# Optimization experiments

Hardware: AMD Instinct MI355X
Metric: run time of the kernel (lower is better)

Reference implementation:

```python
import jax, jax.numpy as jnp
import numpy as np

TEMPERATURE = 0.5
SCALE_LOSS = 1.0 / 32.0
LAMBDA = 0.0039


def setup_inputs() -> dict:
    key = jax.random.key(0)
    z = jax.random.normal(key, (4096, 6, 256), dtype=jnp.float32)
    return {"z": z}


def reference(z):
    B, V = z.shape[0], z.shape[1]
    # [B, V, ...] -> [V, B, D], L2-normalize embeddings
    zv = z.reshape(B, V, -1).transpose(1, 0, 2)
    zn = zv / jnp.linalg.norm(zv, axis=-1, keepdims=True)

    # Positive error: per-sample cross-view similarity [B, V, V]
    sim_pos = jnp.einsum('vbd,wbd->bvw', zn, zn)
    pos = jnp.exp((1.0 - sim_pos) / TEMPERATURE).mean(axis=(1, 2))  # [B]

    # Negative error: per-view within-batch similarity [V, B, B]
    sim_neg = jnp.exp(jnp.einsum('vbd,vcd->vbc', zn, zn) / TEMPERATURE)
    offdiag_mask = ~jnp.eye(B, dtype=bool)  # [B, B]
    off_mean = jnp.where(offdiag_mask[None], sim_neg, 0.0).sum(-1) / (B - 1)  # [V, B]
    neg = off_mean.sum(0)  # [B], accumulated over views

    return jnp.sum(pos) * SCALE_LOSS + LAMBDA * jnp.sum(neg)
```

## Files before the change

### kernel.cpp

```cpp
#include <hip/hip_runtime.h>
#include <cstdint>
#include <cstddef>

#define B_N 4096
#define V_N 6
#define D_N 256
#define CHUNK 8
#define NCHUNK 80
#define NGRAM (NCHUNK * V_N)
#define NPOSB 1024

typedef int i32x4 __attribute__((ext_vector_type(4)));

#define QC 298.0f
#define INV_C2_X2 (2.0f / (QC * QC))

__device__ __forceinline__ void async_load16(void* lds, const void* gmem) {
  __builtin_amdgcn_global_load_lds(
      (const __attribute__((address_space(1))) unsigned int*)gmem,
      (__attribute__((address_space(3))) unsigned int*)lds,
      16, 0, 0);
}

__global__ __launch_bounds__(256) void norm_pos_kernel(
    const float* __restrict__ z, signed char* __restrict__ znb,
    float* __restrict__ pos_blk, int* __restrict__ done) {
  const int lane = threadIdx.x & 63;
  const int w = threadIdx.x >> 6;
  const int b = blockIdx.x * 4 + w;
  __shared__ float red[4];

  if (blockIdx.x == 0 && threadIdx.x == 0) *done = 0;

  const float4* zb4 = (const float4*)(z + (size_t)b * (V_N * D_N));
  float4 x[V_N];
#pragma unroll
  for (int v = 0; v < V_N; ++v) x[v] = zb4[v * 64 + lane];

  float s[21];
  {
    int p = 0;
#pragma unroll
    for (int v = 0; v < V_N; ++v)
#pragma unroll
      for (int u = v; u < V_N; ++u) {
        s[p] = x[v].x * x[u].x + x[v].y * x[u].y +
               x[v].z * x[u].z + x[v].w * x[u].w;
        ++p;
      }
  }
#pragma unroll
  for (int off = 1; off < 64; off <<= 1)
#pragma unroll
    for (int q = 0; q < 21; ++q)
      s[q] += __shfl_xor(s[q], off);

  const int selfidx[V_N] = {0, 6, 11, 15, 18, 20};
  float inv[V_N];
#pragma unroll
  for (int v = 0; v < V_N; ++v) inv[v] = rsqrtf(s[selfidx[v]]);

#pragma unroll
  for (int v = 0; v < V_N; ++v) {
    const float sc = inv[v] * QC;
    int q0 = (int)rintf(fminf(127.0f, fmaxf(-127.0f, x[v].x * sc)));
    int q1 = (int)rintf(fminf(127.0f, fmaxf(-127.0f, x[v].y * sc)));
    int q2 = (int)rintf(fminf(127.0f, fmaxf(-127.0f, x[v].z * sc)));
    int q3 = (int)rintf(fminf(127.0f, fmaxf(-127.0f, x[v].w * sc)));
    int packed = (q0 & 255) | ((q1 & 255) << 8) | ((q2 & 255) << 16)
               | ((q3 & 255) << 24);
    ((int*)(znb + ((size_t)v * B_N + b) * D_N))[lane] = packed;
  }

  float psum = 0.0f;
  {
    int p = 0;
#pragma unroll
    for (int v = 0; v < V_N; ++v)
#pragma unroll
      for (int u = v; u < V_N; ++u) {
        if (u > v) psum += __expf(2.0f * (1.0f - s[p] * inv[v] * inv[u]));
        ++p;
      }
  }
  if (lane == 0) red[w] = psum;
  __syncthreads();
  if (threadIdx.x == 0)
    pos_blk[blockIdx.x] = red[0] + red[1] + red[2] + red[3];
}

__global__ __launch_bounds__(256, 2) void gram_kernel(
    const signed char* __restrict__ znb, const float* __restrict__ pos_blk,
    float* __restrict__ neg_blk, int* __restrict__ done,
    float* __restrict__ out) {
  const int v = blockIdx.y;
  const int bid = blockIdx.y * NCHUNK + blockIdx.x;

  int i = 31, rem = blockIdx.x;
  for (int r = 31; r >= 0; --r) {
    const int nc = (r + 8) >> 3;
    if (rem < nc) { i = r; break; }
    rem -= nc;
  }
  const int j0 = rem * CHUNK;
  const int jend = min(j0 + CHUNK, i + 1);
  const int nsteps = 2 * (jend - j0);

  const signed char* Zv = znb + (size_t)v * B_N * D_N;
  const signed char* Ag = Zv + (size_t)(i * 128) * D_N;

  __shared__ signed char As[128][256];
  __shared__ signed char Bs[2][128][128];
  __shared__ float red[4];
  __shared__ int lastblk;

  const int tid = threadIdx.x;
  const int lane = tid & 63;
  const int w = tid >> 6;
  const int wr = w >> 1;
  const int wc = w & 1;
  const int kc = lane >> 4;
  const int mrow = wr * 64 + (lane & 15);
  const int ncol = wc * 64 + (lane & 15);

  signed char* AsF = &As[0][0];

#pragma unroll
  for (int q = 0; q < 8; ++q) {
    const int sA = tid + 256 * q;
    const int row = sA >> 4;
    const int gc = (sA & 15) ^ (row & 15);
    async_load16(AsF + sA * 16, Ag + (size_t)row * D_N + gc * 16);
  }
#pragma unroll
  for (int st = 0; st < 2; ++st) {
    if (st < nsteps) {
      const int jn = j0 + (st >> 1), hn = st & 1;
      const signed char* Bg = Zv + (size_t)(jn * 128) * D_N + hn * 128;
      signed char* BsF = &Bs[st & 1][0][0];
#pragma unroll
      for (int q = 0; q < 4; ++q) {
        const int s = tid + 256 * q;
        const int row = s >> 3;
        const int gc = (s & 7) ^ (row & 7);
        async_load16(BsF + s * 16, Bg + (size_t)row * D_N + gc * 16);
      }
    }
  }
  asm volatile("s_waitcnt vmcnt(4)" ::: "memory");
  __builtin_amdgcn_sched_barrier(0);
  __builtin_amdgcn_s_barrier();

  float wsum = 0.0f;
  int s = 0;
  for (int jt = j0; jt < jend; ++jt) {
    i32x4 c[4][4];
#pragma unroll
    for (int a = 0; a < 4; ++a)
#pragma unroll
      for (int b2 = 0; b2 < 4; ++b2) c[a][b2] = (i32x4){0, 0, 0, 0};

#pragma unroll
    for (int h = 0; h < 2; ++h, ++s) {
      const signed char* BsF = &Bs[s & 1][0][0];
      __builtin_amdgcn_s_setprio(1);
#pragma unroll
      for (int kk = 0; kk < 2; ++kk) {
        const int cb8 = kk * 4 + kc;
        const int ca16 = h * 8 + kk * 4 + kc;
        i32x4 af[4], bfr[4];
#pragma unroll
        for (int f = 0; f < 4; ++f) {
          const int ra = mrow + 16 * f;
          const int rb = ncol + 16 * f;
          af[f]  = *(const i32x4*)(AsF + ra * 256 + ((ca16 ^ (ra & 15)) * 16));
          bfr[f] = *(const i32x4*)(BsF + rb * 128 + ((cb8 ^ (rb & 7)) * 16));
        }
#pragma unroll
        for (int fm = 0; fm < 4; ++fm)
#pragma unroll
          for (int fn = 0; fn < 4; ++fn)
            c[fm][fn] = __builtin_amdgcn_mfma_i32_16x16x64_i8(
                af[fm], bfr[fn], c[fm][fn], 0, 0, 0);
      }
      __builtin_amdgcn_s_setprio(0);
      __builtin_amdgcn_s_barrier();
      const int sn = s + 2;
      if (sn < nsteps) {
        const int jn = j0 + (sn >> 1), hn = sn & 1;
        const signed char* Bg = Zv + (size_t)(jn * 128) * D_N + hn * 128;
        signed char* BsN = &Bs[s & 1][0][0];
#pragma unroll
        for (int q = 0; q < 4; ++q) {
          const int sg = tid + 256 * q;
          const int row = sg >> 3;
          const int gc = (sg & 7) ^ (row & 7);
          async_load16(BsN + sg * 16, Bg + (size_t)row * D_N + gc * 16);
        }
      }
      if (h == 1) {
        float tsum = 0.0f;
        if (i != jt) {
#pragma unroll
          for (int fm = 0; fm < 4; ++fm)
#pragma unroll
            for (int fn = 0; fn < 4; ++fn)
#pragma unroll
              for (int r = 0; r < 4; ++r)
                tsum += __expf((float)c[fm][fn][r] * INV_C2_X2);
          wsum += 2.0f * tsum;
        } else {
          const int rb0 = wr * 64 + (lane >> 4) * 4;
          const int cb0 = wc * 64 + (lane & 15);
#pragma unroll
          for (int fm = 0; fm < 4; ++fm)
#pragma unroll
            for (int fn = 0; fn < 4; ++fn) {
              const int gcol = cb0 + fn * 16;
#pragma unroll
              for (int r = 0; r < 4; ++r) {
                const int grow = rb0 + fm * 16 + r;
                float e = __expf((float)c[fm][fn][r] * INV_C2_X2);
                tsum += (grow == gcol) ? 0.0f : e;
              }
            }
          wsum += tsum;
        }
      }
      if (sn < nsteps) {
        asm volatile("s_waitcnt vmcnt(4)" ::: "memory");
      } else {
        asm volatile("s_waitcnt vmcnt(0)" ::: "memory");
      }
      __builtin_amdgcn_sched_barrier(0);
      __builtin_amdgcn_s_barrier();
    }
  }

#pragma unroll
  for (int off = 32; off > 0; off >>= 1) wsum += __shfl_down(wsum, off);
  if (lane == 0) red[w] = wsum;
  __syncthreads();
  if (tid == 0) {
    neg_blk[bid] = red[0] + red[1] + red[2] + red[3];
    __threadfence();
    lastblk = (atomicAdd(done, 1) == NGRAM - 1) ? 1 : 0;
  }
  __syncthreads();

  if (lastblk) {
    float p = 0.0f, n = 0.0f;
    for (int idx = tid; idx < NPOSB; idx += 256) p += pos_blk[idx];
    for (int idx = tid; idx < NGRAM; idx += 256)
      n += __hip_atomic_load(&neg_blk[idx], __ATOMIC_RELAXED,
                             __HIP_MEMORY_SCOPE_AGENT);
#pragma unroll
    for (int off = 32; off > 0; off >>= 1) {
      p += __shfl_down(p, off);
      n += __shfl_down(n, off);
    }
    __shared__ float pr[4], nr[4];
    if (lane == 0) { pr[w] = p; nr[w] = n; }
    __syncthreads();
    if (tid == 0) {
      float P = pr[0] + pr[1] + pr[2] + pr[3];
      float N = nr[0] + nr[1] + nr[2] + nr[3];
      out[0] = (1.0f / 32.0f) * ((float)B_N / 6.0f + P / 18.0f) +
               0.0039f * (N / (float)(B_N - 1));
    }
  }
}

extern "C" void kernel_launch(void* const* d_in, const int* in_sizes, int n_in,
                              void* d_out, int out_size, void* d_ws, size_t ws_size,
                              hipStream_t stream) {
  const float* z = (const float*)d_in[0];
  float* out = (float*)d_out;
  float* pos_blk = (float*)d_ws;
  float* neg_blk = (float*)((char*)d_ws + 8192);
  int* done = (int*)((char*)d_ws + 16384);
  signed char* znb = (signed char*)((char*)d_ws + 32768);

  norm_pos_kernel<<<NPOSB, 256, 0, stream>>>(z, znb, pos_blk, done);
  dim3 grid(NCHUNK, V_N, 1);
  gram_kernel<<<grid, 256, 0, stream>>>(znb, pos_blk, neg_blk, done, out);
}
```

Before: 108.5 us.

## Fuse normalize and gram kernels into one persistent kernel with grid barrier

Merges the normalization/positive-term kernel and the int8 gram kernel into a single launch of 480 blocks. Each block does a grid-strided share of normalization, then waits on a global atomic barrier before running its gram tile. Monotonic device counters replace the per-launch reset. This removes a kernel launch and the gap between the two kernels, but requires all 480 blocks to be co-resident (2 per CU) or the barrier deadlocks. The first phase now runs with fewer blocks and more iterations each.

```diff
diff --git a/kernel.cpp b/kernel.cpp
--- a/kernel.cpp
+++ b/kernel.cpp
@@ -8,12 +8,14 @@
 #define CHUNK 8
 #define NCHUNK 80
 #define NGRAM (NCHUNK * V_N)
-#define NPOSB 1024
 
 typedef int i32x4 __attribute__((ext_vector_type(4)));
 
 #define QC 298.0f
 #define INV_C2_X2 (2.0f / (QC * QC))
+
+__device__ int g_bar = 0;
+__device__ int g_fin = 0;
 
 __device__ __forceinline__ void async_load16(void* lds, const void* gmem) {
   __builtin_amdgcn_global_load_lds(
@@ -22,81 +24,94 @@
       16, 0, 0);
 }
 
-__global__ __launch_bounds__(256) void norm_pos_kernel(
+__global__ __launch_bounds__(256, 2) void mega_kernel(
     const float* __restrict__ z, signed char* __restrict__ znb,
-    float* __restrict__ pos_blk, int* __restrict__ done) {
-  const int lane = threadIdx.x & 63;
-  const int w = threadIdx.x >> 6;
-  const int b = blockIdx.x * 4 + w;
+    float* __restrict__ pos_blk, float* __restrict__ neg_blk,
+    float* __restrict__ out) {
+  __shared__ signed char As[128][256];
+  __shared__ signed char Bs[2][128][128];
   __shared__ float red[4];
-
-  if (blockIdx.x == 0 && threadIdx.x == 0) *done = 0;
-
-  const float4* zb4 = (const float4*)(z + (size_t)b * (V_N * D_N));
-  float4 x[V_N];
-#pragma unroll
-  for (int v = 0; v < V_N; ++v) x[v] = zb4[v * 64 + lane];
-
-  float s[21];
-  {
-    int p = 0;
-#pragma unroll
-    for (int v = 0; v < V_N; ++v)
-#pragma unroll
-      for (int u = v; u < V_N; ++u) {
-        s[p] = x[v].x * x[u].x + x[v].y * x[u].y +
-               x[v].z * x[u].z + x[v].w * x[u].w;
-        ++p;
-      }
-  }
-#pragma unroll
-  for (int off = 1; off < 64; off <<= 1)
-#pragma unroll
-    for (int q = 0; q < 21; ++q)
-      s[q] += __shfl_xor(s[q], off);
-
-  const int selfidx[V_N] = {0, 6, 11, 15, 18, 20};
-  float inv[V_N];
-#pragma unroll
-  for (int v = 0; v < V_N; ++v) inv[v] = rsqrtf(s[selfidx[v]]);
-
-#pragma unroll
-  for (int v = 0; v < V_N; ++v) {
-    const float sc = inv[v] * QC;
-    int q0 = (int)rintf(fminf(127.0f, fmaxf(-127.0f, x[v].x * sc)));
-    int q1 = (int)rintf(fminf(127.0f, fmaxf(-127.0f, x[v].y * sc)));
-    int q2 = (int)rintf(fminf(127.0f, fmaxf(-127.0f, x[v].z * sc)));
-    int q3 = (int)rintf(fminf(127.0f, fmaxf(-127.0f, x[v].w * sc)));
-    int packed = (q0 & 255) | ((q1 & 255) << 8) | ((q2 & 255) << 16)
-               | ((q3 & 255) << 24);
-    ((int*)(znb + ((size_t)v * B_N + b) * D_N))[lane] = packed;
-  }
-
-  float psum = 0.0f;
-  {
-    int p = 0;
-#pragma unroll
-    for (int v = 0; v < V_N; ++v)
-#pragma unroll
-      for (int u = v; u < V_N; ++u) {
-        if (u > v) psum += __expf(2.0f * (1.0f - s[p] * inv[v] * inv[u]));
-        ++p;
-      }
-  }
-  if (lane == 0) red[w] = psum;
-  __syncthreads();
-  if (threadIdx.x == 0)
-    pos_blk[blockIdx.x] = red[0] + red[1] + red[2] + red[3];
-}
-
-__global__ __launch_bounds__(256, 2) void gram_kernel(
-    const signed char* __restrict__ znb, const float* __restrict__ pos_blk,
-    float* __restrict__ neg_blk, int* __restrict__ done,
-    float* __restrict__ out) {
-  const int v = blockIdx.y;
-  const int bid = blockIdx.y * NCHUNK + blockIdx.x;
-
-  int i = 31, rem = blockIdx.x;
+  __shared__ float pr[4], nr[4];
+  __shared__ int lastblk;
+
+  const int bx = blockIdx.x;
+  const int tid = threadIdx.x;
+  const int lane = tid & 63;
+  const int w = tid >> 6;
+
+  float pacc = 0.0f;
+  for (int b = bx * 4 + w; b < B_N; b += NGRAM * 4) {
+    const float4* zb4 = (const float4*)(z + (size_t)b * (V_N * D_N));
+    float4 x[V_N];
+#pragma unroll
+    for (int v = 0; v < V_N; ++v) x[v] = zb4[v * 64 + lane];
+
+    float s[21];
+    {
+      int p = 0;
+#pragma unroll
+      for (int v = 0; v < V_N; ++v)
+#pragma unroll
+        for (int u = v; u < V_N; ++u) {
+          s[p] = x[v].x * x[u].x + x[v].y * x[u].y +
+                 x[v].z * x[u].z + x[v].w * x[u].w;
+          ++p;
+        }
+    }
+#pragma unroll
+    for (int off = 1; off < 64; off <<= 1)
+#pragma unroll
+      for (int q = 0; q < 21; ++q)
+        s[q] += __shfl_xor(s[q], off);
+
+    const int selfidx[V_N] = {0, 6, 11, 15, 18, 20};
+    float inv[V_N];
+#pragma unroll
+    for (int v = 0; v < V_N; ++v) inv[v] = rsqrtf(s[selfidx[v]]);
+
+#pragma unroll
+    for (int v = 0; v < V_N; ++v) {
+      const float sc = inv[v] * QC;
+      int q0 = (int)rintf(fminf(127.0f, fmaxf(-127.0f, x[v].x * sc)));
+      int q1 = (int)rintf(fminf(127.0f, fmaxf(-127.0f, x[v].y * sc)));
+      int q2 = (int)rintf(fminf(127.0f, fmaxf(-127.0f, x[v].z * sc)));
+      int q3 = (int)rintf(fminf(127.0f, fmaxf(-127.0f, x[v].w * sc)));
+      int packed = (q0 & 255) | ((q1 & 255) << 8) | ((q2 & 255) << 16)
+                 | ((q3 & 255) << 24);
+      ((int*)(znb + ((size_t)v * B_N + b) * D_N))[lane] = packed;
+    }
+
+    {
+      int p = 0;
+#pragma unroll
+      for (int v = 0; v < V_N; ++v)
+#pragma unroll
+        for (int u = v; u < V_N; ++u) {
+          if (u > v) pacc += __expf(2.0f * (1.0f - s[p] * inv[v] * inv[u]));
+          ++p;
+        }
+    }
+  }
+  if (lane == 0) red[w] = pacc;
+  __syncthreads();
+  if (tid == 0) pos_blk[bx] = red[0] + red[1] + red[2] + red[3];
+
+  if (tid == 0) {
+    __threadfence();
+    int ticket = __hip_atomic_fetch_add(&g_bar, 1, __ATOMIC_ACQ_REL,
+                                        __HIP_MEMORY_SCOPE_AGENT);
+    const int target = (ticket / NGRAM + 1) * NGRAM;
+    while (__hip_atomic_load(&g_bar, __ATOMIC_ACQUIRE,
+                             __HIP_MEMORY_SCOPE_AGENT) < target)
+      __builtin_amdgcn_s_sleep(1);
+  }
+  __syncthreads();
+  __threadfence();
+
+  const int v = bx / NCHUNK;
+  const int cid = bx % NCHUNK;
+
+  int i = 31, rem = cid;
   for (int r = 31; r >= 0; --r) {
     const int nc = (r + 8) >> 3;
     if (rem < nc) { i = r; break; }
@@ -109,14 +124,6 @@
   const signed char* Zv = znb + (size_t)v * B_N * D_N;
   const signed char* Ag = Zv + (size_t)(i * 128) * D_N;
 
-  __shared__ signed char As[128][256];
-  __shared__ signed char Bs[2][128][128];
-  __shared__ float red[4];
-  __shared__ int lastblk;
-
-  const int tid = threadIdx.x;
-  const int lane = tid & 63;
-  const int w = tid >> 6;
   const int wr = w >> 1;
   const int wc = w & 1;
   const int kc = lane >> 4;
@@ -242,24 +249,27 @@
   if (lane == 0) red[w] = wsum;
   __syncthreads();
   if (tid == 0) {
-    neg_blk[bid] = red[0] + red[1] + red[2] + red[3];
+    neg_blk[bx] = red[0] + red[1] + red[2] + red[3];
     __threadfence();
-    lastblk = (atomicAdd(done, 1) == NGRAM - 1) ? 1 : 0;
+    int t2 = __hip_atomic_fetch_add(&g_fin, 1, __ATOMIC_ACQ_REL,
+                                    __HIP_MEMORY_SCOPE_AGENT);
+    lastblk = ((t2 % NGRAM) == NGRAM - 1) ? 1 : 0;
   }
   __syncthreads();
 
   if (lastblk) {
     float p = 0.0f, n = 0.0f;
-    for (int idx = tid; idx < NPOSB; idx += 256) p += pos_blk[idx];
-    for (int idx = tid; idx < NGRAM; idx += 256)
+    for (int idx = tid; idx < NGRAM; idx += 256) {
+      p += __hip_atomic_load(&pos_blk[idx], __ATOMIC_RELAXED,
+                             __HIP_MEMORY_SCOPE_AGENT);
       n += __hip_atomic_load(&neg_blk[idx], __ATOMIC_RELAXED,
                              __HIP_MEMORY_SCOPE_AGENT);
+    }
 #pragma unroll
     for (int off = 32; off > 0; off >>= 1) {
       p += __shfl_down(p, off);
       n += __shfl_down(n, off);
     }
-    __shared__ float pr[4], nr[4];
     if (lane == 0) { pr[w] = p; nr[w] = n; }
     __syncthreads();
     if (tid == 0) {
@@ -278,10 +288,7 @@
   float* out = (float*)d_out;
   float* pos_blk = (float*)d_ws;
   float* neg_blk = (float*)((char*)d_ws + 8192);
-  int* done = (int*)((char*)d_ws + 16384);
   signed char* znb = (signed char*)((char*)d_ws + 32768);
 
-  norm_pos_kernel<<<NPOSB, 256, 0, stream>>>(z, znb, pos_blk, done);
-  dim3 grid(NCHUNK, V_N, 1);
-  gram_kernel<<<grid, 256, 0, stream>>>(znb, pos_blk, neg_blk, done, out);
+  mega_kernel<<<NGRAM, 256, 0, stream>>>(z, znb, pos_blk, neg_blk, out);
 }
```

Result: slower. 206.4 us (+90.2%).
